# Kernel optimization log

Hardware: AMD Instinct MI355X
Metric: run time of the kernel (lower is better)

## Reference

```python
import jax, jax.numpy as jnp
import numpy as np

B, N, D = 8, 1024, 1024
E, H = 16, 4096
CAP_FACTOR = 1.25  # training-mode capacity factor
NUM_CLASSES = 345


def setup_inputs() -> dict:
    key = jax.random.key(0)
    k1, k2, k3, k4 = jax.random.split(key, 4)
    inputs = jax.random.normal(k1, (B, N, D), dtype=jnp.float32)
    current_y = jax.random.randint(k2, (B,), 0, NUM_CLASSES, dtype=jnp.int32)
    std1 = 1.0 / np.sqrt(H)  # init_ uses 1/sqrt(last dim)
    std2 = 1.0 / np.sqrt(D)
    w1 = jax.random.uniform(k3, (E, D, H), dtype=jnp.float32, minval=-std1, maxval=std1)
    w2 = jax.random.uniform(k4, (E, H, D), dtype=jnp.float32, minval=-std2, maxval=std2)
    return {"inputs": inputs, "current_y": current_y, "w1": w1, "w2": w2}


def reference(inputs, current_y, w1, w2):
    b, n, d = inputs.shape
    e = w1.shape[0]
    cap = max(min(n, int(n * CAP_FACTOR / e)), 4)  # MIN_EXPERT_CAPACITY=4
    dt = inputs.dtype

    # class-based gating: every token of sample i goes to expert y_i % e
    idx = jnp.broadcast_to(jnp.remainder(current_y, e)[:, None], (b, n))  # (b,n)
    oh = jax.nn.one_hot(idx, e, dtype=dt)                                 # (b,n,e)
    # exclusive cumsum over token dim, masked
    pos = (jnp.cumsum(oh, axis=-2) - oh) * oh                             # (b,n,e)
    mask1 = oh * (pos < cap).astype(dt)                                   # drop overflow tokens
    mask1_flat = mask1.sum(axis=-1)                                       # (b,n)
    pos_flat = pos.sum(axis=-1).astype(jnp.int32)                         # (b,n)

    # combine[b,n,e,c]; out-of-range positions -> zero row (safe_one_hot semantics)
    combine = (mask1_flat[..., None, None]
               * oh[..., None]
               * jax.nn.one_hot(pos_flat, cap, dtype=dt)[..., None, :])
    dispatch = (combine > 0).astype(dt)

    # dispatch tokens to padded expert slots: (e, b, cap, d)
    expert_in = jnp.einsum('bnd,bnec->ebcd', inputs, dispatch).reshape(e, b * cap, d)
    hidden = jax.nn.gelu(jnp.einsum('end,edh->enh', expert_in, w1), approximate=False)
    expert_out = jnp.einsum('enh,ehd->end', hidden, w2).reshape(e, b, cap, d)

    output = jnp.einsum('ebcd,bnec->bnd', expert_out, combine)
    return output
```

## Files before the change

kernel.cpp:

```cpp
#include <hip/hip_runtime.h>
#include <hip/hip_bf16.h>

#define NB   8
#define NTOK 1024
#define DDIM 1024
#define NEXP 16
#define HDIM 4096
#define CAP  80
#define BK   64
#define BN   128
#define LDA  (BK + 8)

using bf16x8 = __attribute__((ext_vector_type(8))) __bf16;
using bf16x4 = __attribute__((ext_vector_type(4))) __bf16;
using f32x4  = __attribute__((ext_vector_type(4))) float;

__global__ __launch_bounds__(512) void moe_g1(
    const float* __restrict__ X, const int* __restrict__ Y,
    const float* __restrict__ W1, float* __restrict__ Hpart)
{
    const int b     = blockIdx.y;
    const int e     = Y[b] & (NEXP - 1);
    const int nbase = blockIdx.x * BN;
    const int kz    = blockIdx.z * 512;
    const int tid   = threadIdx.x;
    const int w     = tid >> 6;
    const int l     = tid & 63;
    const int q     = l >> 4;
    const int r     = l & 15;
    const int n     = nbase + w * 16 + r;
    const int kb    = tid & 15;
    const int hb    = tid >> 4;

    __shared__ __bf16 As[2][CAP][LDA];
    __shared__ __bf16 Bt[2][BN][LDA];

    const float* Xb  = X  + (size_t)b * NTOK * DDIM;
    const float* W1e = W1 + (size_t)e * DDIM * HDIM;

    f32x4 acc[5];
    #pragma unroll
    for (int i = 0; i < 5; ++i) acc[i] = f32x4{0.f, 0.f, 0.f, 0.f};

    float4 a_reg[3];
    float4 b_reg[4];

    #pragma unroll
    for (int it = 0; it < 3; ++it) {
        int idx = tid + 512 * it;
        if (it < 2 || idx < CAP * 16) {
            int row = idx >> 4, kg = idx & 15;
            a_reg[it] = *(const float4*)&Xb[(size_t)row * DDIM + kz + kg * 4];
        }
    }
    #pragma unroll
    for (int kk = 0; kk < 4; ++kk)
        b_reg[kk] = *(const float4*)&W1e[(size_t)(kz + kb * 4 + kk) * HDIM + nbase + hb * 4];

    int cur = 0;
    for (int t = 0; t < 8; ++t) {
        #pragma unroll
        for (int it = 0; it < 3; ++it) {
            int idx = tid + 512 * it;
            if (it < 2 || idx < CAP * 16) {
                int row = idx >> 4, kg = idx & 15;
                float4 v = a_reg[it];
                bf16x4 p = {(__bf16)v.x, (__bf16)v.y, (__bf16)v.z, (__bf16)v.w};
                *(bf16x4*)&As[cur][row][kg * 4] = p;
            }
        }
        {
            bf16x4 p0 = {(__bf16)b_reg[0].x, (__bf16)b_reg[1].x, (__bf16)b_reg[2].x, (__bf16)b_reg[3].x};
            bf16x4 p1 = {(__bf16)b_reg[0].y, (__bf16)b_reg[1].y, (__bf16)b_reg[2].y, (__bf16)b_reg[3].y};
            bf16x4 p2 = {(__bf16)b_reg[0].z, (__bf16)b_reg[1].z, (__bf16)b_reg[2].z, (__bf16)b_reg[3].z};
            bf16x4 p3 = {(__bf16)b_reg[0].w, (__bf16)b_reg[1].w, (__bf16)b_reg[2].w, (__bf16)b_reg[3].w};
            *(bf16x4*)&Bt[cur][hb * 4 + 0][kb * 4] = p0;
            *(bf16x4*)&Bt[cur][hb * 4 + 1][kb * 4] = p1;
            *(bf16x4*)&Bt[cur][hb * 4 + 2][kb * 4] = p2;
            *(bf16x4*)&Bt[cur][hb * 4 + 3][kb * 4] = p3;
        }
        __syncthreads();

        if (t + 1 < 8) {
            const int k0 = kz + (t + 1) * BK;
            #pragma unroll
            for (int it = 0; it < 3; ++it) {
                int idx = tid + 512 * it;
                if (it < 2 || idx < CAP * 16) {
                    int row = idx >> 4, kg = idx & 15;
                    a_reg[it] = *(const float4*)&Xb[(size_t)row * DDIM + k0 + kg * 4];
                }
            }
            #pragma unroll
            for (int kk = 0; kk < 4; ++kk)
                b_reg[kk] = *(const float4*)&W1e[(size_t)(k0 + kb * 4 + kk) * HDIM + nbase + hb * 4];
        }

        #pragma unroll
        for (int s = 0; s < 2; ++s) {
            bf16x8 bf = *(const bf16x8*)&Bt[cur][w * 16 + r][s * 32 + q * 8];
            #pragma unroll
            for (int mt = 0; mt < 5; ++mt) {
                bf16x8 af = *(const bf16x8*)&As[cur][mt * 16 + r][s * 32 + q * 8];
                acc[mt] = __builtin_amdgcn_mfma_f32_16x16x32_bf16(af, bf, acc[mt], 0, 0, 0);
            }
        }
        cur ^= 1;
    }

    float* Hp = Hpart + ((size_t)blockIdx.z * NB + b) * CAP * HDIM;
    #pragma unroll
    for (int mt = 0; mt < 5; ++mt)
        #pragma unroll
        for (int v = 0; v < 4; ++v) {
            int m = mt * 16 + q * 4 + v;
            Hp[(size_t)m * HDIM + n] = acc[mt][v];
        }
}

__global__ __launch_bounds__(256) void gelu_red(const float* __restrict__ Hpart,
                                                __bf16* __restrict__ Hid)
{
    size_t i4 = (size_t)blockIdx.x * 256 + threadIdx.x;
    const size_t SL = (size_t)NB * CAP * HDIM;
    float4 v0 = *(const float4*)&Hpart[i4 * 4];
    float4 v1 = *(const float4*)&Hpart[SL + i4 * 4];
    float s[4] = {v0.x + v1.x, v0.y + v1.y, v0.z + v1.z, v0.w + v1.w};
    bf16x4 p;
    #pragma unroll
    for (int j = 0; j < 4; ++j) {
        float x = s[j];
        p[j] = (__bf16)(0.5f * x * (1.0f + erff(x * 0.70710678118654752f)));
    }
    *(bf16x4*)&Hid[i4 * 4] = p;
}

__global__ __launch_bounds__(512) void moe_g2(
    const __bf16* __restrict__ Hid, const int* __restrict__ Y,
    const float* __restrict__ W2, float* __restrict__ Opart)
{
    const int b     = blockIdx.y;
    const int e     = Y[b] & (NEXP - 1);
    const int nbase = blockIdx.x * BN;
    const int kz    = blockIdx.z * 512;
    const int tid   = threadIdx.x;
    const int w     = tid >> 6;
    const int l     = tid & 63;
    const int q     = l >> 4;
    const int r     = l & 15;
    const int n     = nbase + w * 16 + r;
    const int kb    = tid & 15;
    const int hb    = tid >> 4;

    __shared__ __bf16 As[2][CAP][LDA];
    __shared__ __bf16 Bt[2][BN][LDA];

    const __bf16* Hb  = Hid + (size_t)b * CAP * HDIM;
    const float*  W2e = W2  + (size_t)e * HDIM * DDIM;

    f32x4 acc[5];
    #pragma unroll
    for (int i = 0; i < 5; ++i) acc[i] = f32x4{0.f, 0.f, 0.f, 0.f};

    uint2  a_reg[3];
    float4 b_reg[4];

    #pragma unroll
    for (int it = 0; it < 3; ++it) {
        int idx = tid + 512 * it;
        if (it < 2 || idx < CAP * 16) {
            int row = idx >> 4, kg = idx & 15;
            a_reg[it] = *(const uint2*)&Hb[(size_t)row * HDIM + kz + kg * 4];
        }
    }
    #pragma unroll
    for (int kk = 0; kk < 4; ++kk)
        b_reg[kk] = *(const float4*)&W2e[(size_t)(kz + kb * 4 + kk) * DDIM + nbase + hb * 4];

    int cur = 0;
    for (int t = 0; t < 8; ++t) {
        #pragma unroll
        for (int it = 0; it < 3; ++it) {
            int idx = tid + 512 * it;
            if (it < 2 || idx < CAP * 16) {
                int row = idx >> 4, kg = idx & 15;
                *(uint2*)&As[cur][row][kg * 4] = a_reg[it];
            }
        }
        {
            bf16x4 p0 = {(__bf16)b_reg[0].x, (__bf16)b_reg[1].x, (__bf16)b_reg[2].x, (__bf16)b_reg[3].x};
            bf16x4 p1 = {(__bf16)b_reg[0].y, (__bf16)b_reg[1].y, (__bf16)b_reg[2].y, (__bf16)b_reg[3].y};
            bf16x4 p2 = {(__bf16)b_reg[0].z, (__bf16)b_reg[1].z, (__bf16)b_reg[2].z, (__bf16)b_reg[3].z};
            bf16x4 p3 = {(__bf16)b_reg[0].w, (__bf16)b_reg[1].w, (__bf16)b_reg[2].w, (__bf16)b_reg[3].w};
            *(bf16x4*)&Bt[cur][hb * 4 + 0][kb * 4] = p0;
            *(bf16x4*)&Bt[cur][hb * 4 + 1][kb * 4] = p1;
            *(bf16x4*)&Bt[cur][hb * 4 + 2][kb * 4] = p2;
            *(bf16x4*)&Bt[cur][hb * 4 + 3][kb * 4] = p3;
        }
        __syncthreads();

        if (t + 1 < 8) {
            const int k0 = kz + (t + 1) * BK;
            #pragma unroll
            for (int it = 0; it < 3; ++it) {
                int idx = tid + 512 * it;
                if (it < 2 || idx < CAP * 16) {
                    int row = idx >> 4, kg = idx & 15;
                    a_reg[it] = *(const uint2*)&Hb[(size_t)row * HDIM + k0 + kg * 4];
                }
            }
            #pragma unroll
            for (int kk = 0; kk < 4; ++kk)
                b_reg[kk] = *(const float4*)&W2e[(size_t)(k0 + kb * 4 + kk) * DDIM + nbase + hb * 4];
        }

        #pragma unroll
        for (int s = 0; s < 2; ++s) {
            bf16x8 bf = *(const bf16x8*)&Bt[cur][w * 16 + r][s * 32 + q * 8];
            #pragma unroll
            for (int mt = 0; mt < 5; ++mt) {
                bf16x8 af = *(const bf16x8*)&As[cur][mt * 16 + r][s * 32 + q * 8];
                acc[mt] = __builtin_amdgcn_mfma_f32_16x16x32_bf16(af, bf, acc[mt], 0, 0, 0);
            }
        }
        cur ^= 1;
    }

    float* Op = Opart + ((size_t)blockIdx.z * NB + b) * CAP * DDIM;
    #pragma unroll
    for (int mt = 0; mt < 5; ++mt)
        #pragma unroll
        for (int v = 0; v < 4; ++v) {
            int m = mt * 16 + q * 4 + v;
            Op[(size_t)m * DDIM + n] = acc[mt][v];
        }
}

__global__ __launch_bounds__(256) void out_red(const float* __restrict__ Opart,
                                               float* __restrict__ Out)
{
    size_t i4 = (size_t)blockIdx.x * 256 + threadIdx.x;
    const size_t SL = (size_t)NB * CAP * DDIM;
    float4 s = *(const float4*)&Opart[i4 * 4];
    #pragma unroll
    for (int z = 1; z < 8; ++z) {
        float4 v = *(const float4*)&Opart[(size_t)z * SL + i4 * 4];
        s.x += v.x; s.y += v.y; s.z += v.z; s.w += v.w;
    }
    size_t i = i4 * 4;
    size_t b = i / ((size_t)CAP * DDIM);
    size_t rem = i % ((size_t)CAP * DDIM);
    size_t m = rem / DDIM, d = rem % DDIM;
    *(float4*)&Out[(b * NTOK + m) * DDIM + d] = s;
}

extern "C" void kernel_launch(void* const* d_in, const int* in_sizes, int n_in,
                              void* d_out, int out_size, void* d_ws, size_t ws_size,
                              hipStream_t stream) {
    const float* X  = (const float*)d_in[0];
    const int*   Y  = (const int*)d_in[1];
    const float* W1 = (const float*)d_in[2];
    const float* W2 = (const float*)d_in[3];
    float* Out = (float*)d_out;

    uint8_t* ws = (uint8_t*)d_ws;
    __bf16* Hid   = (__bf16*)ws;
    float*  Hpart = (float*)(ws + (8u  << 20));
    float*  Opart = (float*)(ws + (32u << 20));

    hipMemsetAsync(d_out, 0, (size_t)out_size * sizeof(float), stream);

    moe_g1<<<dim3(HDIM / BN, NB, 2), 512, 0, stream>>>(X, Y, W1, Hpart);
    gelu_red<<<dim3(NB * CAP * HDIM / 4 / 256), 256, 0, stream>>>(Hpart, Hid);
    moe_g2<<<dim3(DDIM / BN, NB, 8), 512, 0, stream>>>(Hid, Y, W2, Opart);
    out_red<<<dim3(NB * CAP * DDIM / 4 / 256), 256, 0, stream>>>(Opart, Out);
}
```

Baseline: 492.0 us.

## Load weight fragments directly from global memory and widen per-wave N tile

Both GEMM kernels stop staging the fp32 weights through shared memory. Each wave now reads its bf16 MFMA B fragments straight from global memory with strided scalar loads and covers a 64-column N tile, holding 5x4 accumulators. Block N width grows to 512 and the split-K factor rises to 4 and 16, so the reduction kernels sum more partial slices. This removes the LDS transpose traffic and the B-side register prefetch. In exchange it adds uncoalesced scalar global loads, more partial-sum traffic and higher register pressure.

```diff
diff --git a/kernel.cpp b/kernel.cpp
--- a/kernel.cpp
+++ b/kernel.cpp
@@ -8,7 +8,6 @@
 #define HDIM 4096
 #define CAP  80
 #define BK   64
-#define BN   128
 #define LDA  (BK + 8)
 
 using bf16x8 = __attribute__((ext_vector_type(8))) __bf16;
@@ -19,32 +18,29 @@
     const float* __restrict__ X, const int* __restrict__ Y,
     const float* __restrict__ W1, float* __restrict__ Hpart)
 {
-    const int b     = blockIdx.y;
-    const int e     = Y[b] & (NEXP - 1);
-    const int nbase = blockIdx.x * BN;
-    const int kz    = blockIdx.z * 512;
-    const int tid   = threadIdx.x;
-    const int w     = tid >> 6;
-    const int l     = tid & 63;
-    const int q     = l >> 4;
-    const int r     = l & 15;
-    const int n     = nbase + w * 16 + r;
-    const int kb    = tid & 15;
-    const int hb    = tid >> 4;
+    const int b   = blockIdx.y;
+    const int e   = Y[b] & (NEXP - 1);
+    const int hc  = blockIdx.x;
+    const int kz  = blockIdx.z * 256;
+    const int tid = threadIdx.x;
+    const int w   = tid >> 6;
+    const int l   = tid & 63;
+    const int q   = l >> 4;
+    const int r   = l & 15;
+    const int n0  = hc * 512 + w * 64;
 
     __shared__ __bf16 As[2][CAP][LDA];
-    __shared__ __bf16 Bt[2][BN][LDA];
 
     const float* Xb  = X  + (size_t)b * NTOK * DDIM;
     const float* W1e = W1 + (size_t)e * DDIM * HDIM;
 
-    f32x4 acc[5];
-    #pragma unroll
-    for (int i = 0; i < 5; ++i) acc[i] = f32x4{0.f, 0.f, 0.f, 0.f};
+    f32x4 acc[5][4];
+    #pragma unroll
+    for (int i = 0; i < 5; ++i)
+        #pragma unroll
+        for (int j = 0; j < 4; ++j) acc[i][j] = f32x4{0.f, 0.f, 0.f, 0.f};
 
     float4 a_reg[3];
-    float4 b_reg[4];
-
     #pragma unroll
     for (int it = 0; it < 3; ++it) {
         int idx = tid + 512 * it;
@@ -53,12 +49,11 @@
             a_reg[it] = *(const float4*)&Xb[(size_t)row * DDIM + kz + kg * 4];
         }
     }
-    #pragma unroll
-    for (int kk = 0; kk < 4; ++kk)
-        b_reg[kk] = *(const float4*)&W1e[(size_t)(kz + kb * 4 + kk) * HDIM + nbase + hb * 4];
 
     int cur = 0;
-    for (int t = 0; t < 8; ++t) {
+    for (int t = 0; t < 4; ++t) {
+        const int k0 = kz + t * BK;
+
         #pragma unroll
         for (int it = 0; it < 3; ++it) {
             int idx = tid + 512 * it;
@@ -69,53 +64,52 @@
                 *(bf16x4*)&As[cur][row][kg * 4] = p;
             }
         }
-        {
-            bf16x4 p0 = {(__bf16)b_reg[0].x, (__bf16)b_reg[1].x, (__bf16)b_reg[2].x, (__bf16)b_reg[3].x};
-            bf16x4 p1 = {(__bf16)b_reg[0].y, (__bf16)b_reg[1].y, (__bf16)b_reg[2].y, (__bf16)b_reg[3].y};
-            bf16x4 p2 = {(__bf16)b_reg[0].z, (__bf16)b_reg[1].z, (__bf16)b_reg[2].z, (__bf16)b_reg[3].z};
-            bf16x4 p3 = {(__bf16)b_reg[0].w, (__bf16)b_reg[1].w, (__bf16)b_reg[2].w, (__bf16)b_reg[3].w};
-            *(bf16x4*)&Bt[cur][hb * 4 + 0][kb * 4] = p0;
-            *(bf16x4*)&Bt[cur][hb * 4 + 1][kb * 4] = p1;
-            *(bf16x4*)&Bt[cur][hb * 4 + 2][kb * 4] = p2;
-            *(bf16x4*)&Bt[cur][hb * 4 + 3][kb * 4] = p3;
-        }
-        __syncthreads();
-
-        if (t + 1 < 8) {
-            const int k0 = kz + (t + 1) * BK;
+        __syncthreads();
+
+        if (t + 1 < 4) {
+            const int kn = kz + (t + 1) * BK;
             #pragma unroll
             for (int it = 0; it < 3; ++it) {
                 int idx = tid + 512 * it;
                 if (it < 2 || idx < CAP * 16) {
                     int row = idx >> 4, kg = idx & 15;
-                    a_reg[it] = *(const float4*)&Xb[(size_t)row * DDIM + k0 + kg * 4];
-                }
-            }
-            #pragma unroll
-            for (int kk = 0; kk < 4; ++kk)
-                b_reg[kk] = *(const float4*)&W1e[(size_t)(k0 + kb * 4 + kk) * HDIM + nbase + hb * 4];
+                    a_reg[it] = *(const float4*)&Xb[(size_t)row * DDIM + kn + kg * 4];
+                }
+            }
         }
 
         #pragma unroll
         for (int s = 0; s < 2; ++s) {
-            bf16x8 bf = *(const bf16x8*)&Bt[cur][w * 16 + r][s * 32 + q * 8];
-            #pragma unroll
-            for (int mt = 0; mt < 5; ++mt) {
-                bf16x8 af = *(const bf16x8*)&As[cur][mt * 16 + r][s * 32 + q * 8];
-                acc[mt] = __builtin_amdgcn_mfma_f32_16x16x32_bf16(af, bf, acc[mt], 0, 0, 0);
-            }
-        }
+            #pragma unroll
+            for (int nt = 0; nt < 4; ++nt) {
+                const float* bp = W1e + (size_t)(k0 + s * 32 + q * 8) * HDIM + n0 + nt * 16 + r;
+                float bv[8];
+                #pragma unroll
+                for (int j = 0; j < 8; ++j) bv[j] = bp[(size_t)j * HDIM];
+                bf16x8 bf;
+                #pragma unroll
+                for (int j = 0; j < 8; ++j) bf[j] = (__bf16)bv[j];
+                #pragma unroll
+                for (int mt = 0; mt < 5; ++mt) {
+                    bf16x8 af = *(const bf16x8*)&As[cur][mt * 16 + r][s * 32 + q * 8];
+                    acc[mt][nt] = __builtin_amdgcn_mfma_f32_16x16x32_bf16(af, bf, acc[mt][nt], 0, 0, 0);
+                }
+            }
+        }
+        __syncthreads();
         cur ^= 1;
     }
 
-    float* Hp = Hpart + ((size_t)blockIdx.z * NB + b) * CAP * HDIM;
+    float* Hp = Hpart + ((size_t)(blockIdx.z * NB + b) * CAP) * HDIM;
     #pragma unroll
     for (int mt = 0; mt < 5; ++mt)
         #pragma unroll
-        for (int v = 0; v < 4; ++v) {
-            int m = mt * 16 + q * 4 + v;
-            Hp[(size_t)m * HDIM + n] = acc[mt][v];
-        }
+        for (int nt = 0; nt < 4; ++nt)
+            #pragma unroll
+            for (int v = 0; v < 4; ++v) {
+                int m = mt * 16 + q * 4 + v;
+                Hp[(size_t)m * HDIM + n0 + nt * 16 + r] = acc[mt][nt][v];
+            }
 }
 
 __global__ __launch_bounds__(256) void gelu_red(const float* __restrict__ Hpart,
@@ -123,13 +117,17 @@
 {
     size_t i4 = (size_t)blockIdx.x * 256 + threadIdx.x;
     const size_t SL = (size_t)NB * CAP * HDIM;
-    float4 v0 = *(const float4*)&Hpart[i4 * 4];
-    float4 v1 = *(const float4*)&Hpart[SL + i4 * 4];
-    float s[4] = {v0.x + v1.x, v0.y + v1.y, v0.z + v1.z, v0.w + v1.w};
+    float4 s = *(const float4*)&Hpart[i4 * 4];
+    #pragma unroll
+    for (int z = 1; z < 4; ++z) {
+        float4 v = *(const float4*)&Hpart[(size_t)z * SL + i4 * 4];
+        s.x += v.x; s.y += v.y; s.z += v.z; s.w += v.w;
+    }
+    float a[4] = {s.x, s.y, s.z, s.w};
     bf16x4 p;
     #pragma unroll
     for (int j = 0; j < 4; ++j) {
-        float x = s[j];
+        float x = a[j];
         p[j] = (__bf16)(0.5f * x * (1.0f + erff(x * 0.70710678118654752f)));
     }
     *(bf16x4*)&Hid[i4 * 4] = p;
@@ -139,32 +137,29 @@
     const __bf16* __restrict__ Hid, const int* __restrict__ Y,
     const float* __restrict__ W2, float* __restrict__ Opart)
 {
-    const int b     = blockIdx.y;
-    const int e     = Y[b] & (NEXP - 1);
-    const int nbase = blockIdx.x * BN;
-    const int kz    = blockIdx.z * 512;
-    const int tid   = threadIdx.x;
-    const int w     = tid >> 6;
-    const int l     = tid & 63;
-    const int q     = l >> 4;
-    const int r     = l & 15;
-    const int n     = nbase + w * 16 + r;
-    const int kb    = tid & 15;
-    const int hb    = tid >> 4;
+    const int b   = blockIdx.y;
+    const int e   = Y[b] & (NEXP - 1);
+    const int dc  = blockIdx.x;
+    const int kz  = blockIdx.z * 256;
+    const int tid = threadIdx.x;
+    const int w   = tid >> 6;
+    const int l   = tid & 63;
+    const int q   = l >> 4;
+    const int r   = l & 15;
+    const int n0  = dc * 512 + w * 64;
 
     __shared__ __bf16 As[2][CAP][LDA];
-    __shared__ __bf16 Bt[2][BN][LDA];
 
     const __bf16* Hb  = Hid + (size_t)b * CAP * HDIM;
     const float*  W2e = W2  + (size_t)e * HDIM * DDIM;
 
-    f32x4 acc[5];
-    #pragma unroll
-    for (int i = 0; i < 5; ++i) acc[i] = f32x4{0.f, 0.f, 0.f, 0.f};
-
-    uint2  a_reg[3];
-    float4 b_reg[4];
-
+    f32x4 acc[5][4];
+    #pragma unroll
+    for (int i = 0; i < 5; ++i)
+        #pragma unroll
+        for (int j = 0; j < 4; ++j) acc[i][j] = f32x4{0.f, 0.f, 0.f, 0.f};
+
+    uint2 a_reg[3];
     #pragma unroll
     for (int it = 0; it < 3; ++it) {
         int idx = tid + 512 * it;
@@ -173,12 +168,11 @@
             a_reg[it] = *(const uint2*)&Hb[(size_t)row * HDIM + kz + kg * 4];
         }
     }
-    #pragma unroll
-    for (int kk = 0; kk < 4; ++kk)
-        b_reg[kk] = *(const float4*)&W2e[(size_t)(kz + kb * 4 + kk) * DDIM + nbase + hb * 4];
 
     int cur = 0;
-    for (int t = 0; t < 8; ++t) {
+    for (int t = 0; t < 4; ++t) {
+        const int k0 = kz + t * BK;
+
         #pragma unroll
         for (int it = 0; it < 3; ++it) {
             int idx = tid + 512 * it;
@@ -187,53 +181,52 @@
                 *(uint2*)&As[cur][row][kg * 4] = a_reg[it];
             }
         }
-        {
-            bf16x4 p0 = {(__bf16)b_reg[0].x, (__bf16)b_reg[1].x, (__bf16)b_reg[2].x, (__bf16)b_reg[3].x};
-            bf16x4 p1 = {(__bf16)b_reg[0].y, (__bf16)b_reg[1].y, (__bf16)b_reg[2].y, (__bf16)b_reg[3].y};
-            bf16x4 p2 = {(__bf16)b_reg[0].z, (__bf16)b_reg[1].z, (__bf16)b_reg[2].z, (__bf16)b_reg[3].z};
-            bf16x4 p3 = {(__bf16)b_reg[0].w, (__bf16)b_reg[1].w, (__bf16)b_reg[2].w, (__bf16)b_reg[3].w};
-            *(bf16x4*)&Bt[cur][hb * 4 + 0][kb * 4] = p0;
-            *(bf16x4*)&Bt[cur][hb * 4 + 1][kb * 4] = p1;
-            *(bf16x4*)&Bt[cur][hb * 4 + 2][kb * 4] = p2;
-            *(bf16x4*)&Bt[cur][hb * 4 + 3][kb * 4] = p3;
-        }
-        __syncthreads();
-
-        if (t + 1 < 8) {
-            const int k0 = kz + (t + 1) * BK;
+        __syncthreads();
+
+        if (t + 1 < 4) {
+            const int kn = kz + (t + 1) * BK;
             #pragma unroll
             for (int it = 0; it < 3; ++it) {
                 int idx = tid + 512 * it;
                 if (it < 2 || idx < CAP * 16) {
                     int row = idx >> 4, kg = idx & 15;
-                    a_reg[it] = *(const uint2*)&Hb[(size_t)row * HDIM + k0 + kg * 4];
-                }
-            }
-            #pragma unroll
-            for (int kk = 0; kk < 4; ++kk)
-                b_reg[kk] = *(const float4*)&W2e[(size_t)(k0 + kb * 4 + kk) * DDIM + nbase + hb * 4];
+                    a_reg[it] = *(const uint2*)&Hb[(size_t)row * HDIM + kn + kg * 4];
+                }
+            }
         }
 
         #pragma unroll
         for (int s = 0; s < 2; ++s) {
-            bf16x8 bf = *(const bf16x8*)&Bt[cur][w * 16 + r][s * 32 + q * 8];
-            #pragma unroll
-            for (int mt = 0; mt < 5; ++mt) {
-                bf16x8 af = *(const bf16x8*)&As[cur][mt * 16 + r][s * 32 + q * 8];
-                acc[mt] = __builtin_amdgcn_mfma_f32_16x16x32_bf16(af, bf, acc[mt], 0, 0, 0);
-            }
-        }
+            #pragma unroll
+            for (int nt = 0; nt < 4; ++nt) {
+                const float* bp = W2e + (size_t)(k0 + s * 32 + q * 8) * DDIM + n0 + nt * 16 + r;
+                float bv[8];
+                #pragma unroll
+                for (int j = 0; j < 8; ++j) bv[j] = bp[(size_t)j * DDIM];
+                bf16x8 bf;
+                #pragma unroll
+                for (int j = 0; j < 8; ++j) bf[j] = (__bf16)bv[j];
+                #pragma unroll
+                for (int mt = 0; mt < 5; ++mt) {
+                    bf16x8 af = *(const bf16x8*)&As[cur][mt * 16 + r][s * 32 + q * 8];
+                    acc[mt][nt] = __builtin_amdgcn_mfma_f32_16x16x32_bf16(af, bf, acc[mt][nt], 0, 0, 0);
+                }
+            }
+        }
+        __syncthreads();
         cur ^= 1;
     }
 
-    float* Op = Opart + ((size_t)blockIdx.z * NB + b) * CAP * DDIM;
+    float* Op = Opart + ((size_t)(blockIdx.z * NB + b) * CAP) * DDIM;
     #pragma unroll
     for (int mt = 0; mt < 5; ++mt)
         #pragma unroll
-        for (int v = 0; v < 4; ++v) {
-            int m = mt * 16 + q * 4 + v;
-            Op[(size_t)m * DDIM + n] = acc[mt][v];
-        }
+        for (int nt = 0; nt < 4; ++nt)
+            #pragma unroll
+            for (int v = 0; v < 4; ++v) {
+                int m = mt * 16 + q * 4 + v;
+                Op[(size_t)m * DDIM + n0 + nt * 16 + r] = acc[mt][nt][v];
+            }
 }
 
 __global__ __launch_bounds__(256) void out_red(const float* __restrict__ Opart,
@@ -243,7 +236,7 @@
     const size_t SL = (size_t)NB * CAP * DDIM;
     float4 s = *(const float4*)&Opart[i4 * 4];
     #pragma unroll
-    for (int z = 1; z < 8; ++z) {
+    for (int z = 1; z < 16; ++z) {
         float4 v = *(const float4*)&Opart[(size_t)z * SL + i4 * 4];
         s.x += v.x; s.y += v.y; s.z += v.z; s.w += v.w;
     }
@@ -266,12 +259,12 @@
     uint8_t* ws = (uint8_t*)d_ws;
     __bf16* Hid   = (__bf16*)ws;
     float*  Hpart = (float*)(ws + (8u  << 20));
-    float*  Opart = (float*)(ws + (32u << 20));
+    float*  Opart = (float*)(ws + (64u << 20));
 
     hipMemsetAsync(d_out, 0, (size_t)out_size * sizeof(float), stream);
 
-    moe_g1<<<dim3(HDIM / BN, NB, 2), 512, 0, stream>>>(X, Y, W1, Hpart);
+    moe_g1<<<dim3(HDIM / 512, NB, 4),  512, 0, stream>>>(X, Y, W1, Hpart);
     gelu_red<<<dim3(NB * CAP * HDIM / 4 / 256), 256, 0, stream>>>(Hpart, Hid);
-    moe_g2<<<dim3(DDIM / BN, NB, 8), 512, 0, stream>>>(Hid, Y, W2, Opart);
+    moe_g2<<<dim3(DDIM / 512, NB, 16), 512, 0, stream>>>(Hid, Y, W2, Opart);
     out_red<<<dim3(NB * CAP * DDIM / 4 / 256), 256, 0, stream>>>(Opart, Out);
 }
```

Result: slower. 504.0 us (+2.4%).
